# Kernel tuning notes

Measured on AMD Instinct MI355X. Metric: run time of the kernel, lower is better.

The kernel has to match this reference:

```python
import jax, jax.numpy as jnp
import numpy as np

B, T, C = 4, 2048, 768
N_HEAD = 12
HS = C // N_HEAD

def setup_inputs() -> dict:
    key = jax.random.key(0)
    ks = jax.random.split(key, 5)
    s = 0.02
    return {
        "x": jax.random.normal(ks[0], (B, T, C), dtype=jnp.float32),
        "w_attn": jax.random.normal(ks[1], (C, 3 * C), dtype=jnp.float32) * s,
        "b_attn": jnp.zeros((3 * C,), dtype=jnp.float32),
        "w_proj": jax.random.normal(ks[2], (C, C), dtype=jnp.float32) * s,
        "b_proj": jnp.zeros((C,), dtype=jnp.float32),
    }

def reference(x, w_attn, b_attn, w_proj, b_proj):
    Bx, Tx, Cx = x.shape
    qkv = x @ w_attn + b_attn                      # [B,T,3C]
    q, k, v = jnp.split(qkv, 3, axis=-1)
    # [B,H,T,hs]
    q = q.reshape(Bx, Tx, N_HEAD, HS).transpose(0, 2, 1, 3)
    k = k.reshape(Bx, Tx, N_HEAD, HS).transpose(0, 2, 1, 3)
    v = v.reshape(Bx, Tx, N_HEAD, HS).transpose(0, 2, 1, 3)
    att = jnp.einsum('bhqd,bhkd->bhqk', q, k) * (1.0 / jnp.sqrt(jnp.float32(HS)))
    mask = jnp.tril(jnp.ones((Tx, Tx), dtype=bool))  # causal
    att = jnp.where(mask, att, jnp.float32(-jnp.inf))
    att = jax.nn.softmax(att, axis=-1)
    y = jnp.einsum('bhqk,bhkd->bhqd', att, v)
    y = y.transpose(0, 2, 1, 3).reshape(Bx, Tx, Cx)
    return y @ w_proj + b_proj
```

## Files before the change

### kernel.cpp

```cpp
#include <hip/hip_runtime.h>

#define BB 4
#define TT 2048
#define CC 768
#define QKVW 2304
#define NHH 12
#define HSS 64
#define NQT64 (TT / 64)

typedef __attribute__((ext_vector_type(4))) float floatx4;
typedef __attribute__((ext_vector_type(8))) short shortx8;
typedef __attribute__((ext_vector_type(4))) short shortx4;

__device__ __forceinline__ unsigned short f2bf(float f) {
  union { float f; unsigned int u; } cv; cv.f = f;
  unsigned int u = cv.u;
  u += 0x7FFFu + ((u >> 16) & 1u);
  return (unsigned short)(u >> 16);
}
__device__ __forceinline__ unsigned short bfp(float f) {
  union { float f; unsigned int u; } cv; cv.f = f;
  return (unsigned short)((cv.u + 0x8000u) >> 16);
}
__device__ __forceinline__ unsigned short bft(float f) {
  union { float f; unsigned int u; } cv; cv.f = f;
  return (unsigned short)(cv.u >> 16);
}

__device__ __forceinline__ void async_copy16(const void* g, void* l) {
  __builtin_amdgcn_global_load_lds(
      (const __attribute__((address_space(1))) unsigned int*)g,
      (__attribute__((address_space(3))) unsigned int*)l, 16, 0, 0);
}

__global__ void convert_x(const float* __restrict__ x, unsigned short* __restrict__ xb, int n4) {
  int i = blockIdx.x * blockDim.x + threadIdx.x;
  const int stride = gridDim.x * blockDim.x;
  for (; i < n4; i += stride) {
    float4 v = ((const float4*)x)[i];
    shortx4 s;
    s.x = (short)f2bf(v.x); s.y = (short)f2bf(v.y);
    s.z = (short)f2bf(v.z); s.w = (short)f2bf(v.w);
    ((shortx4*)xb)[i] = s;
  }
}

__global__ __launch_bounds__(256)
void transpose_w(const float* __restrict__ w, unsigned short* __restrict__ wt, int K, int N) {
  __shared__ short tile[64 * 68];
  const int n0 = blockIdx.x * 64, k0 = blockIdx.y * 64;
  const int tid = threadIdx.x;
  {
    const int tr = tid >> 4, tc = (tid & 15) * 4;
#pragma unroll
    for (int i = 0; i < 4; ++i) {
      float4 v = *(const float4*)(w + (size_t)(k0 + tr + 16 * i) * N + n0 + tc);
      short* d = &tile[(tr + 16 * i) * 68 + tc];
      d[0] = (short)f2bf(v.x); d[1] = (short)f2bf(v.y);
      d[2] = (short)f2bf(v.z); d[3] = (short)f2bf(v.w);
    }
  }
  __syncthreads();
  {
    const int wr = tid >> 3, wc = (tid & 7) * 8;
#pragma unroll
    for (int j = 0; j < 2; ++j) {
      const int n = wr + 32 * j;
      shortx8 s;
#pragma unroll
      for (int e = 0; e < 8; ++e) s[e] = tile[(wc + e) * 68 + n];
      *(shortx8*)(wt + (size_t)(n0 + n) * K + k0 + wc) = s;
    }
  }
}

__global__ __launch_bounds__(256)
void transpose_v(const unsigned short* __restrict__ qkv, unsigned short* __restrict__ Vt) {
  __shared__ short tile[64 * 72];
  const int t0 = blockIdx.x * 64;
  const int bh = blockIdx.y;
  const int b = bh / NHH, h = bh % NHH;
  const int tid = threadIdx.x;
  {
    const int tr = tid >> 3, tc = (tid & 7) * 8;
#pragma unroll
    for (int i = 0; i < 2; ++i) {
      shortx8 v = *(const shortx8*)(qkv + ((size_t)(b * TT + t0 + tr + 32 * i)) * QKVW + 2 * CC + h * HSS + tc);
      *(shortx8*)&tile[(tr + 32 * i) * 72 + tc] = v;
    }
  }
  __syncthreads();
  {
    const int dr = tid >> 3, tc = (tid & 7) * 8;
    const int base = (tc & 32) + ((tc >> 3) & 3) * 4;
#pragma unroll
    for (int j = 0; j < 2; ++j) {
      const int d = dr + 32 * j;
      shortx8 s;
#pragma unroll
      for (int e = 0; e < 8; ++e)
        s[e] = tile[(base + (e >> 2) * 16 + (e & 3)) * 72 + d];
      *(shortx8*)(Vt + ((size_t)bh * HSS + d) * TT + t0 + tc) = s;
    }
  }
}

template<bool OUT_BF16, bool QSCALE>
__global__ __launch_bounds__(256)
void gemm_tn(const unsigned short* __restrict__ A, const unsigned short* __restrict__ Bt,
             const float* __restrict__ bias, void* __restrict__ Cp, int M, int N, int K) {
  __shared__ short As0[128 * 32], As1[128 * 32];
  __shared__ short Bs0[128 * 32], Bs1[128 * 32];
  const int tid = threadIdx.x, lane = tid & 63, wave = tid >> 6;
  const int row = lane & 15, quad = lane >> 4;
  const int wm = (wave >> 1) * 64, wn = (wave & 1) * 64;
  const int m0 = blockIdx.x * 128, n0 = blockIdx.y * 128;

  floatx4 acc[4][4] = {};

  const int sr = wave * 32 + (lane >> 2);
  const int sc = (lane & 3) * 8;
  const unsigned short* aP = A + (size_t)(m0 + sr) * K + sc;
  const unsigned short* bP = Bt + (size_t)(n0 + sr) * K + sc;
  short* as0Base = &As0[(wave * 32) * 32];
  short* as1Base = &As1[(wave * 32) * 32];
  short* bs0Base = &Bs0[(wave * 32) * 32];
  short* bs1Base = &Bs1[(wave * 32) * 32];

  for (int k0 = 0; k0 < K; k0 += 64) {
#pragma unroll
    for (int i = 0; i < 2; ++i) {
      async_copy16(aP + (size_t)(16 * i) * K + k0,      as0Base + i * 512);
      async_copy16(aP + (size_t)(16 * i) * K + k0 + 32, as1Base + i * 512);
      async_copy16(bP + (size_t)(16 * i) * K + k0,      bs0Base + i * 512);
      async_copy16(bP + (size_t)(16 * i) * K + k0 + 32, bs1Base + i * 512);
    }
    __syncthreads();
    {
      shortx8 af[4], bf[4];
#pragma unroll
      for (int g = 0; g < 4; ++g) {
        af[g] = *(const shortx8*)&As0[(wm + g * 16 + row) * 32 + quad * 8];
        bf[g] = *(const shortx8*)&Bs0[(wn + g * 16 + row) * 32 + quad * 8];
      }
#pragma unroll
      for (int mg = 0; mg < 4; ++mg)
#pragma unroll
        for (int ng = 0; ng < 4; ++ng)
          acc[mg][ng] = __builtin_amdgcn_mfma_f32_16x16x32_bf16(af[mg], bf[ng], acc[mg][ng], 0, 0, 0);
#pragma unroll
      for (int g = 0; g < 4; ++g) {
        af[g] = *(const shortx8*)&As1[(wm + g * 16 + row) * 32 + quad * 8];
        bf[g] = *(const shortx8*)&Bs1[(wn + g * 16 + row) * 32 + quad * 8];
      }
#pragma unroll
      for (int mg = 0; mg < 4; ++mg)
#pragma unroll
        for (int ng = 0; ng < 4; ++ng)
          acc[mg][ng] = __builtin_amdgcn_mfma_f32_16x16x32_bf16(af[mg], bf[ng], acc[mg][ng], 0, 0, 0);
    }
    __syncthreads();
  }

#pragma unroll
  for (int mg = 0; mg < 4; ++mg) {
    const int m = m0 + wm + mg * 16 + quad * 4;
#pragma unroll
    for (int ng = 0; ng < 4; ++ng) {
      const int n = n0 + wn + ng * 16 + row;
      const float bv = bias[n];
      const float scl = (QSCALE && n < CC) ? 0.180336881f : 1.0f;
#pragma unroll
      for (int r = 0; r < 4; ++r) {
        const float val = (acc[mg][ng][r] + bv) * scl;
        if (OUT_BF16) ((unsigned short*)Cp)[(size_t)(m + r) * N + n] = f2bf(val);
        else          ((float*)Cp)[(size_t)(m + r) * N + n] = val;
      }
    }
  }
}

__global__ __launch_bounds__(256)
void attn_kernel(const unsigned short* __restrict__ qkv, const unsigned short* __restrict__ Vt,
                 unsigned short* __restrict__ y) {
  constexpr int STR = 72;
  __shared__ short Kd[2][64 * STR];
  __shared__ short Vd[2][64 * STR];

  const int p = blockIdx.x;
  const int h = blockIdx.y, b = blockIdx.z;
  const int bh = b * NHH + h;
  const int tid = threadIdx.x, lane = tid & 63, wave = tid >> 6;
  const int row = lane & 15, quad = lane >> 4;
  const int qhalf = wave & 1;
  const int khalf = wave >> 1;

  const int srow = tid >> 3;
  const int scol = (tid & 7) * 8;
  const unsigned short* kSrc = qkv + ((size_t)(b * TT)) * QKVW + CC + h * HSS;
  const unsigned short* vSrc = Vt + ((size_t)bh * HSS) * TT;

  const shortx8 ones8 = {(short)0x3F80, (short)0x3F80, (short)0x3F80, (short)0x3F80,
                         (short)0x3F80, (short)0x3F80, (short)0x3F80, (short)0x3F80};

  for (int item = 0; item < 2; ++item) {
    const int qt = item == 0 ? (NQT64 - 1 - p) : p;
    const int qb0 = qt * 64 + qhalf * 32;
    const int nk = qt + 1;

    shortx8 qf[2][2];
#pragma unroll
    for (int qg = 0; qg < 2; ++qg) {
      const unsigned short* qp = qkv + ((size_t)(b * TT) + qb0 + qg * 16 + row) * QKVW + h * HSS;
      qf[qg][0] = *(const shortx8*)(qp + quad * 8);
      qf[qg][1] = *(const shortx8*)(qp + 32 + quad * 8);
    }

    floatx4 lf[2] = {(floatx4)(0.0f), (floatx4)(0.0f)};
    floatx4 o[2][4];
#pragma unroll
    for (int qg = 0; qg < 2; ++qg)
#pragma unroll
      for (int dg = 0; dg < 4; ++dg) o[qg][dg] = (floatx4)(0.0f);

    shortx8 kr[2], vr[2];
#pragma unroll
    for (int i = 0; i < 2; ++i) {
      kr[i] = *(const shortx8*)(kSrc + (size_t)(srow + 32 * i) * QKVW + scol);
      vr[i] = *(const shortx8*)(vSrc + (size_t)(srow + 32 * i) * TT + scol);
    }
#pragma unroll
    for (int i = 0; i < 2; ++i) {
      *(shortx8*)&Kd[0][(srow + 32 * i) * STR + scol] = kr[i];
      *(shortx8*)&Vd[0][(srow + 32 * i) * STR + scol] = vr[i];
    }
    __syncthreads();

    for (int kt = 0; kt < nk; ++kt) {
      const int cur = kt & 1;
      if (kt + 1 < nk) {
#pragma unroll
        for (int i = 0; i < 2; ++i) {
          kr[i] = *(const shortx8*)(kSrc + (size_t)((kt + 1) * 64 + srow + 32 * i) * QKVW + scol);
          vr[i] = *(const shortx8*)(vSrc + (size_t)(srow + 32 * i) * TT + (kt + 1) * 64 + scol);
        }
      }
      {
        const short* Kc = &Kd[cur][0];
        const short* Vc = &Vd[cur][0];
        shortx4 pfr[2][2];
#pragma unroll
        for (int mg = 0; mg < 2; ++mg) {
          const int krow = khalf * 32 + mg * 16 + row;
          const shortx8 kf0 = *(const shortx8*)&Kc[krow * STR + quad * 8];
          const shortx8 kf1 = *(const shortx8*)&Kc[krow * STR + 32 + quad * 8];
#pragma unroll
          for (int qg = 0; qg < 2; ++qg) {
            floatx4 t = __builtin_amdgcn_mfma_f32_16x16x32_bf16(kf0, qf[qg][0], (floatx4)(0.0f), 0, 0, 0);
            t = __builtin_amdgcn_mfma_f32_16x16x32_bf16(kf1, qf[qg][1], t, 0, 0, 0);
            if (kt == qt) {
              const int kg = kt * 64 + khalf * 32 + mg * 16 + quad * 4;
              const int qv = qb0 + qg * 16 + row;
#pragma unroll
              for (int r = 0; r < 4; ++r)
                if (kg + r > qv) t[r] = -1e30f;
            }
            shortx4 pk;
#pragma unroll
            for (int r = 0; r < 4; ++r) pk[r] = (short)bft(__builtin_amdgcn_exp2f(t[r]));
            pfr[qg][mg] = pk;
          }
        }
        shortx8 pk8[2];
#pragma unroll
        for (int qg = 0; qg < 2; ++qg) {
          pk8[qg] = __builtin_shufflevector(pfr[qg][0], pfr[qg][1], 0, 1, 2, 3, 4, 5, 6, 7);
          lf[qg] = __builtin_amdgcn_mfma_f32_16x16x32_bf16(pk8[qg], ones8, lf[qg], 0, 0, 0);
        }
#pragma unroll
        for (int dg = 0; dg < 4; ++dg) {
          const shortx8 vf = *(const shortx8*)&Vc[(dg * 16 + row) * STR + khalf * 32 + quad * 8];
#pragma unroll
          for (int qg = 0; qg < 2; ++qg)
            o[qg][dg] = __builtin_amdgcn_mfma_f32_16x16x32_bf16(pk8[qg], vf, o[qg][dg], 0, 0, 0);
        }
      }
      if (kt + 1 < nk) {
        const int nb = (kt + 1) & 1;
#pragma unroll
        for (int i = 0; i < 2; ++i) {
          *(shortx8*)&Kd[nb][(srow + 32 * i) * STR + scol] = kr[i];
          *(shortx8*)&Vd[nb][(srow + 32 * i) * STR + scol] = vr[i];
        }
      }
      __syncthreads();
    }

    floatx4* red4 = (floatx4*)(&Kd[0][0]);
    const int rbase = (qhalf * 64 + lane) * 11;
    if (khalf) {
#pragma unroll
      for (int qg = 0; qg < 2; ++qg) {
#pragma unroll
        for (int dg = 0; dg < 4; ++dg) red4[rbase + qg * 4 + dg] = o[qg][dg];
        red4[rbase + 8 + qg] = lf[qg];
      }
    }
    __syncthreads();
    if (!khalf) {
#pragma unroll
      for (int qg = 0; qg < 2; ++qg) {
#pragma unroll
        for (int dg = 0; dg < 4; ++dg) o[qg][dg] += red4[rbase + qg * 4 + dg];
        lf[qg] += red4[rbase + 8 + qg];
      }
#pragma unroll
      for (int qg = 0; qg < 2; ++qg) {
#pragma unroll
        for (int r = 0; r < 4; ++r) {
          const float lo = 1.0f / lf[qg][r];
          unsigned short* yp = y + ((size_t)(b * TT) + qb0 + qg * 16 + quad * 4 + r) * CC + h * HSS;
#pragma unroll
          for (int dg = 0; dg < 4; ++dg)
            yp[dg * 16 + row] = bfp(o[qg][dg][r] * lo);
        }
      }
    }
    __syncthreads();
  }
}

extern "C" void kernel_launch(void* const* d_in, const int* in_sizes, int n_in,
                              void* d_out, int out_size, void* d_ws, size_t ws_size,
                              hipStream_t stream) {
  const float* x      = (const float*)d_in[0];
  const float* w_attn = (const float*)d_in[1];
  const float* b_attn = (const float*)d_in[2];
  const float* w_proj = (const float*)d_in[3];
  const float* b_proj = (const float*)d_in[4];
  float* out = (float*)d_out;

  char* ws = (char*)d_ws;
  unsigned short* xb  = (unsigned short*)ws;
  unsigned short* y   = (unsigned short*)ws;
  unsigned short* qkv = (unsigned short*)(ws + 12582912);
  unsigned short* wta = (unsigned short*)(ws + 50331648);
  unsigned short* Vt  = (unsigned short*)(ws + 50331648);
  unsigned short* wtp = (unsigned short*)(ws + 62914560);

  const int M = BB * TT;

  convert_x<<<1024, 256, 0, stream>>>(x, xb, (M * CC) / 4);
  transpose_w<<<dim3(QKVW / 64, CC / 64), 256, 0, stream>>>(w_attn, wta, CC, QKVW);
  transpose_w<<<dim3(CC / 64, CC / 64), 256, 0, stream>>>(w_proj, wtp, CC, CC);

  gemm_tn<true, true><<<dim3(M / 128, QKVW / 128), 256, 0, stream>>>(
      xb, wta, b_attn, (void*)qkv, M, QKVW, CC);

  transpose_v<<<dim3(TT / 64, BB * NHH), 256, 0, stream>>>(qkv, Vt);

  attn_kernel<<<dim3(NQT64 / 2, NHH, BB), 256, 0, stream>>>(qkv, Vt, y);

  gemm_tn<false, false><<<dim3(M / 128, CC / 128), 256, 0, stream>>>(
      y, wtp, b_proj, (void*)out, M, CC, CC);
}
```

Baseline: 216.1 us.

## Triple-buffer GEMM LDS tiles with async prefetch and XOR-swizzled layout

Replaces the load-then-compute GEMM main loop with a three-stage ring buffer. Global-to-LDS copies run two k-steps ahead and are gated with explicit vmcnt waits and raw s_barriers, so memory latency overlaps MFMA work. It also XOR-swizzles the 16-byte chunk column per row to cut LDS bank conflicts on fragment reads. The k-step shrinks from 64 to 32, which doubles the number of barriers per tile, and the hand-written waitcnt values must match the copies in flight.

```diff
diff --git a/kernel.cpp b/kernel.cpp
--- a/kernel.cpp
+++ b/kernel.cpp
@@ -109,8 +109,8 @@
 __global__ __launch_bounds__(256)
 void gemm_tn(const unsigned short* __restrict__ A, const unsigned short* __restrict__ Bt,
              const float* __restrict__ bias, void* __restrict__ Cp, int M, int N, int K) {
-  __shared__ short As0[128 * 32], As1[128 * 32];
-  __shared__ short Bs0[128 * 32], Bs1[128 * 32];
+  __shared__ short As[3][128 * 32];
+  __shared__ short Bs[3][128 * 32];
   const int tid = threadIdx.x, lane = tid & 63, wave = tid >> 6;
   const int row = lane & 15, quad = lane >> 4;
   const int wm = (wave >> 1) * 64, wn = (wave & 1) * 64;
@@ -118,48 +118,58 @@
 
   floatx4 acc[4][4] = {};
 
-  const int sr = wave * 32 + (lane >> 2);
-  const int sc = (lane & 3) * 8;
-  const unsigned short* aP = A + (size_t)(m0 + sr) * K + sc;
-  const unsigned short* bP = Bt + (size_t)(n0 + sr) * K + sc;
-  short* as0Base = &As0[(wave * 32) * 32];
-  short* as1Base = &As1[(wave * 32) * 32];
-  short* bs0Base = &Bs0[(wave * 32) * 32];
-  short* bs1Base = &Bs1[(wave * 32) * 32];
-
-  for (int k0 = 0; k0 < K; k0 += 64) {
+  const int lr = lane >> 2;
+  const int csrc = (lane & 3) ^ ((lr >> 1) & 3);
+  const int sr = wave * 32 + lr;
+  const unsigned short* aP = A + (size_t)(m0 + sr) * K + csrc * 8;
+  const unsigned short* bP = Bt + (size_t)(n0 + sr) * K + csrc * 8;
+  const int sOff = (wave * 32) * 32;
+
+  const int qsw = (quad ^ ((row >> 1) & 3)) * 8;
+
+  const int nk = K >> 5;
+
+  auto stage = [&](int t, int bi) {
 #pragma unroll
     for (int i = 0; i < 2; ++i) {
-      async_copy16(aP + (size_t)(16 * i) * K + k0,      as0Base + i * 512);
-      async_copy16(aP + (size_t)(16 * i) * K + k0 + 32, as1Base + i * 512);
-      async_copy16(bP + (size_t)(16 * i) * K + k0,      bs0Base + i * 512);
-      async_copy16(bP + (size_t)(16 * i) * K + k0 + 32, bs1Base + i * 512);
-    }
-    __syncthreads();
+      async_copy16(aP + (size_t)(16 * i) * K + t * 32, &As[bi][sOff + i * 512]);
+      async_copy16(bP + (size_t)(16 * i) * K + t * 32, &Bs[bi][sOff + i * 512]);
+    }
+  };
+
+  stage(0, 0);
+  if (nk > 1) stage(1, 1);
+  int cb = 0;
+  for (int t = 0; t < nk; ++t) {
+    int pb = cb + 2; if (pb >= 3) pb -= 3;
+    if (t + 2 < nk) {
+      stage(t + 2, pb);
+      asm volatile("s_waitcnt vmcnt(8)" ::: "memory");
+    } else if (t + 1 < nk) {
+      asm volatile("s_waitcnt vmcnt(4)" ::: "memory");
+    } else {
+      asm volatile("s_waitcnt vmcnt(0)" ::: "memory");
+    }
+    __builtin_amdgcn_sched_barrier(0);
+    __builtin_amdgcn_s_barrier();
+    __builtin_amdgcn_sched_barrier(0);
     {
       shortx8 af[4], bf[4];
 #pragma unroll
       for (int g = 0; g < 4; ++g) {
-        af[g] = *(const shortx8*)&As0[(wm + g * 16 + row) * 32 + quad * 8];
-        bf[g] = *(const shortx8*)&Bs0[(wn + g * 16 + row) * 32 + quad * 8];
+        af[g] = *(const shortx8*)&As[cb][(wm + g * 16 + row) * 32 + qsw];
+        bf[g] = *(const shortx8*)&Bs[cb][(wn + g * 16 + row) * 32 + qsw];
       }
 #pragma unroll
       for (int mg = 0; mg < 4; ++mg)
 #pragma unroll
         for (int ng = 0; ng < 4; ++ng)
           acc[mg][ng] = __builtin_amdgcn_mfma_f32_16x16x32_bf16(af[mg], bf[ng], acc[mg][ng], 0, 0, 0);
-#pragma unroll
-      for (int g = 0; g < 4; ++g) {
-        af[g] = *(const shortx8*)&As1[(wm + g * 16 + row) * 32 + quad * 8];
-        bf[g] = *(const shortx8*)&Bs1[(wn + g * 16 + row) * 32 + quad * 8];
-      }
-#pragma unroll
-      for (int mg = 0; mg < 4; ++mg)
-#pragma unroll
-        for (int ng = 0; ng < 4; ++ng)
-          acc[mg][ng] = __builtin_amdgcn_mfma_f32_16x16x32_bf16(af[mg], bf[ng], acc[mg][ng], 0, 0, 0);
-    }
-    __syncthreads();
+    }
+    __builtin_amdgcn_sched_barrier(0);
+    __builtin_amdgcn_s_barrier();
+    __builtin_amdgcn_sched_barrier(0);
+    cb = (cb + 1 == 3) ? 0 : cb + 1;
   }
 
 #pragma unroll
```

New measurement: 208.3 us. 3.6% less time.
